# Kernel optimization log

Measured on AMD Instinct MI355X. Metric: run time of the kernel, lower is better.

## Reference

```python
import jax, jax.numpy as jnp
import numpy as np

B, L, H, D, N, R, K = 1, 2048, 2048, 4096, 16, 128, 4


def setup_inputs() -> dict:
    key = jax.random.key(0)
    ks = jax.random.split(key, 10)
    s = 0.02
    x = jax.random.normal(ks[0], (B, L, H), dtype=jnp.float32)
    W_in = jax.random.normal(ks[1], (H, 2 * D), dtype=jnp.float32) * s
    conv_w = jax.random.normal(ks[2], (K, D), dtype=jnp.float32) * s  # depthwise causal conv
    conv_b = jnp.zeros((D,), dtype=jnp.float32)
    W_x = jax.random.normal(ks[3], (D, R + 2 * N), dtype=jnp.float32) * s
    W_dt = jax.random.normal(ks[4], (R, D), dtype=jnp.float32) * (R ** -0.5)
    # dt bias initialized so softplus(b_dt) ~ dt in [1e-3, 1e-1]
    dt = jnp.exp(jax.random.uniform(ks[5], (D,)) * (np.log(0.1) - np.log(1e-3)) + np.log(1e-3))
    b_dt = dt + jnp.log(-jnp.expm1(-dt))
    A_log = jnp.broadcast_to(jnp.log(jnp.arange(1, N + 1, dtype=jnp.float32)), (D, N))
    D_param = jnp.ones((D,), dtype=jnp.float32)
    W_out = jax.random.normal(ks[6], (D, H), dtype=jnp.float32) * s
    return {"x": x, "W_in": W_in, "conv_w": conv_w, "conv_b": conv_b,
            "W_x": W_x, "W_dt": W_dt, "b_dt": b_dt, "A_log": A_log,
            "D_param": D_param, "W_out": W_out}


def _mamba_fwd(x, W_in, conv_w, conv_b, W_x, W_dt, b_dt, A_log, D_param, W_out):
    silu = jax.nn.silu
    # in_proj then chunk into hidden / gate: [B,L,D] each
    proj = x @ W_in
    hs, gate = jnp.split(proj, 2, axis=-1)
    # causal depthwise conv along sequence (pad K-1 on the left)
    hs_pad = jnp.pad(hs, ((0, 0), (K - 1, 0), (0, 0)))
    conv = sum(hs_pad[:, k:k + L, :] * conv_w[k] for k in range(K)) + conv_b
    hs = silu(conv)  # [B,L,D]
    # ssm parameters
    ssm_p = hs @ W_x  # [B,L,R+2N]
    dt_in, Bm, Cm = jnp.split(ssm_p, [R, R + N], axis=-1)
    dt = jax.nn.softplus(dt_in @ W_dt + b_dt)  # [B,L,D]
    A = -jnp.exp(A_log)  # [D,N]
    dA = jnp.exp(dt[..., None] * A)                       # [B,L,D,N]
    dBu = dt[..., None] * Bm[:, :, None, :] * hs[..., None]  # [B,L,D,N]

    def step(s, inp):
        dA_t, dBu_t, C_t = inp
        s = dA_t * s + dBu_t                 # [B,D,N]
        y = jnp.einsum('bdn,bn->bd', s, C_t)
        return s, y

    s0 = jnp.zeros((B, D, N), dtype=x.dtype)
    xs = (jnp.moveaxis(dA, 1, 0), jnp.moveaxis(dBu, 1, 0), jnp.moveaxis(Cm, 1, 0))
    _, ys = jax.lax.scan(step, s0, xs)       # [L,B,D]
    y = jnp.moveaxis(ys, 0, 1)               # [B,L,D]
    y = y + hs * D_param
    y = y * silu(gate)
    return y @ W_out                          # [B,L,H]


def reference(x, W_in, conv_w, conv_b, W_x, W_dt, b_dt, A_log, D_param, W_out):
    return _mamba_fwd(x, W_in, conv_w, conv_b, W_x, W_dt, b_dt, A_log, D_param, W_out)
```

## Files before the change

### kernel.cpp

```cpp
#include <hip/hip_runtime.h>
#include <hip/hip_bf16.h>

typedef short short8 __attribute__((ext_vector_type(8)));
typedef float floatx4 __attribute__((ext_vector_type(4)));
using bf16 = __hip_bfloat16;

static constexpr int L = 2048, H = 2048, D = 4096, NS = 16, R = 128, KC = 4;
static constexpr int CCH = 64, TCH = L / CCH;
static constexpr int KSP = 16, KCHUNK = 4096 / KSP;
static constexpr int ZOUT = 4, KOUT = 4096 / ZOUT;

__device__ __forceinline__ void g2lds16(const void* g, void* l) {
  __builtin_amdgcn_global_load_lds((const __attribute__((address_space(1))) unsigned int*)g,
                                   (__attribute__((address_space(3))) unsigned int*)l,
                                   16, 0, 0);
}

__global__ void cast_f2b(const float* __restrict__ in, bf16* __restrict__ out, int n) {
  int i = blockIdx.x * 256 + threadIdx.x;
  if (i < n) out[i] = __float2bfloat16(in[i]);
}

__global__ void transpose_cast(const float* __restrict__ in, bf16* __restrict__ out,
                               int Rr, int Cc) {
  __shared__ float tile[32][33];
  int c0 = blockIdx.x * 32, r0 = blockIdx.y * 32;
  int tx = threadIdx.x, ty = threadIdx.y;
#pragma unroll
  for (int i = 0; i < 32; i += 8)
    tile[ty + i][tx] = in[(size_t)(r0 + ty + i) * Cc + (c0 + tx)];
  __syncthreads();
#pragma unroll
  for (int i = 0; i < 32; i += 8)
    out[(size_t)(c0 + ty + i) * Rr + (r0 + tx)] = __float2bfloat16(tile[tx][ty + i]);
}

template <int MODE>
__global__ __launch_bounds__(256) void gemm_async(
    const bf16* __restrict__ A, int lda,
    const bf16* __restrict__ Bt, int ldb,
    float* __restrict__ Cf, bf16* __restrict__ Cb, int ldc, int K) {
  __shared__ short As[128 * 32];
  __shared__ short Bs[128 * 32];
  const int m0 = blockIdx.y * 128, n0 = blockIdx.x * 128;
  const int tid = threadIdx.x;
  const int lane = tid & 63;
  const int wave = tid >> 6;
  const int wm = (wave >> 1) * 64, wn = (wave & 1) * 64;
  const int lr = lane & 15, kq = lane >> 4;
  const int sr = lane >> 2, sc = (lane & 3) * 8;

  const bf16* Ab = A + (size_t)(m0 + wave * 16 + sr) * lda + sc;
  const bf16* Bb = Bt + (size_t)(n0 + wave * 16 + sr) * ldb + sc;
  short* Asw = &As[wave * 16 * 32];
  short* Bsw = &Bs[wave * 16 * 32];

  floatx4 acc[4][4];
#pragma unroll
  for (int i = 0; i < 4; i++)
#pragma unroll
    for (int j = 0; j < 4; j++)
#pragma unroll
      for (int r = 0; r < 4; r++) acc[i][j][r] = 0.f;

  for (int k0 = 0; k0 < K; k0 += 32) {
    __syncthreads();
#pragma unroll
    for (int j = 0; j < 2; j++) {
      g2lds16(Ab + (size_t)j * 64 * lda + k0, Asw + j * 64 * 32);
      g2lds16(Bb + (size_t)j * 64 * ldb + k0, Bsw + j * 64 * 32);
    }
    __syncthreads();
    short8 af[4], bfr[4];
#pragma unroll
    for (int i = 0; i < 4; i++)
      af[i] = *(const short8*)(&As[(wm + i * 16 + lr) * 32 + kq * 8]);
#pragma unroll
    for (int j = 0; j < 4; j++)
      bfr[j] = *(const short8*)(&Bs[(wn + j * 16 + lr) * 32 + kq * 8]);
#pragma unroll
    for (int i = 0; i < 4; i++)
#pragma unroll
      for (int j = 0; j < 4; j++)
        acc[i][j] = __builtin_amdgcn_mfma_f32_16x16x32_bf16(af[i], bfr[j], acc[i][j], 0, 0, 0);
  }

  const int rb = kq * 4;
#pragma unroll
  for (int i = 0; i < 4; i++)
#pragma unroll
    for (int j = 0; j < 4; j++) {
      int col = n0 + wn + j * 16 + lr;
      int row = m0 + wm + i * 16 + rb;
#pragma unroll
      for (int r = 0; r < 4; r++) {
        float v = acc[i][j][r];
        if (MODE == 0) {
          Cf[(size_t)(row + r) * ldc + col] = v;
        } else if (MODE == 1) {
          Cb[(size_t)(row + r) * ldc + col] = __float2bfloat16(v);
        } else {
          if (col < D) Cb[(size_t)(row + r) * D + col] = __float2bfloat16(v);
          else         Cf[(size_t)(row + r) * D + col - D] = v;
        }
      }
    }
}

__global__ __launch_bounds__(256) void gemm_async_splitk(
    const bf16* __restrict__ A, int lda,
    const bf16* __restrict__ Bt, int ldb,
    float* __restrict__ P, int ldc, int kch) {
  __shared__ short As[128 * 32];
  __shared__ short Bs[128 * 32];
  const int m0 = blockIdx.y * 128, n0 = blockIdx.x * 128;
  const int kbeg = blockIdx.z * kch;
  float* C = P + (size_t)blockIdx.z * L * ldc;
  const int tid = threadIdx.x;
  const int lane = tid & 63;
  const int wave = tid >> 6;
  const int wm = (wave >> 1) * 64, wn = (wave & 1) * 64;
  const int lr = lane & 15, kq = lane >> 4;
  const int sr = lane >> 2, sc = (lane & 3) * 8;

  const bf16* Ab = A + (size_t)(m0 + wave * 16 + sr) * lda + sc;
  const bf16* Bb = Bt + (size_t)(n0 + wave * 16 + sr) * ldb + sc;
  short* Asw = &As[wave * 16 * 32];
  short* Bsw = &Bs[wave * 16 * 32];

  floatx4 acc[4][4];
#pragma unroll
  for (int i = 0; i < 4; i++)
#pragma unroll
    for (int j = 0; j < 4; j++)
#pragma unroll
      for (int r = 0; r < 4; r++) acc[i][j][r] = 0.f;

  for (int k0 = kbeg; k0 < kbeg + kch; k0 += 32) {
    __syncthreads();
#pragma unroll
    for (int j = 0; j < 2; j++) {
      g2lds16(Ab + (size_t)j * 64 * lda + k0, Asw + j * 64 * 32);
      g2lds16(Bb + (size_t)j * 64 * ldb + k0, Bsw + j * 64 * 32);
    }
    __syncthreads();
    short8 af[4], bfr[4];
#pragma unroll
    for (int i = 0; i < 4; i++)
      af[i] = *(const short8*)(&As[(wm + i * 16 + lr) * 32 + kq * 8]);
#pragma unroll
    for (int j = 0; j < 4; j++)
      bfr[j] = *(const short8*)(&Bs[(wn + j * 16 + lr) * 32 + kq * 8]);
#pragma unroll
    for (int i = 0; i < 4; i++)
#pragma unroll
      for (int j = 0; j < 4; j++)
        acc[i][j] = __builtin_amdgcn_mfma_f32_16x16x32_bf16(af[i], bfr[j], acc[i][j], 0, 0, 0);
  }

  const int rb = kq * 4;
#pragma unroll
  for (int i = 0; i < 4; i++)
#pragma unroll
    for (int j = 0; j < 4; j++) {
      int col = n0 + wn + j * 16 + lr;
      int row = m0 + wm + i * 16 + rb;
#pragma unroll
      for (int r = 0; r < 4; r++)
        C[(size_t)(row + r) * ldc + col] = acc[i][j][r];
    }
}

__global__ void out_reduce(const float* __restrict__ P, float* __restrict__ out) {
  int i = blockIdx.x * 256 + threadIdx.x;
  const int LH4 = L * H / 4;
  const floatx4* P4 = (const floatx4*)P;
  floatx4 s = P4[i];
#pragma unroll
  for (int z = 1; z < ZOUT; z++) s += P4[(size_t)z * LH4 + i];
  ((floatx4*)out)[i] = s;
}

__global__ __launch_bounds__(256) void gemm_splitk(
    const bf16* __restrict__ A, int lda,
    const bf16* __restrict__ Bt, int ldb,
    float* __restrict__ P, int ldc, int N) {
  __shared__ short As[128 * 40];
  __shared__ short Bs[128 * 40];
  const int m0 = blockIdx.y * 128, n0 = blockIdx.x * 128;
  const int kbeg = blockIdx.z * KCHUNK;
  float* C = P + (size_t)blockIdx.z * L * ldc;
  const int tid = threadIdx.x;
  const int lane = tid & 63;
  const int wave = tid >> 6;
  const int wm = (wave >> 1) * 64, wn = (wave & 1) * 64;
  const int lr = lane & 15, kq = lane >> 4;
  const int srow = tid >> 2, scol = (tid & 3) * 8;

  floatx4 acc[4][4];
#pragma unroll
  for (int i = 0; i < 4; i++)
#pragma unroll
    for (int j = 0; j < 4; j++)
#pragma unroll
      for (int r = 0; r < 4; r++) acc[i][j][r] = 0.f;

  for (int k0 = kbeg; k0 < kbeg + KCHUNK; k0 += 32) {
    __syncthreads();
#pragma unroll
    for (int h = 0; h < 2; h++) {
      int r = srow + h * 64;
      short8 va = *(const short8*)((const short*)A + (size_t)(m0 + r) * lda + k0 + scol);
      *(short8*)(&As[r * 40 + scol]) = va;
    }
#pragma unroll
    for (int h = 0; h < 2; h++) {
      int r = srow + h * 64;
      short8 vb;
      if ((n0 + r) < N) {
        vb = *(const short8*)((const short*)Bt + (size_t)(n0 + r) * ldb + k0 + scol);
      } else {
#pragma unroll
        for (int q = 0; q < 8; q++) vb[q] = 0;
      }
      *(short8*)(&Bs[r * 40 + scol]) = vb;
    }
    __syncthreads();
    short8 af[4], bfr[4];
#pragma unroll
    for (int i = 0; i < 4; i++)
      af[i] = *(const short8*)(&As[(wm + i * 16 + lr) * 40 + kq * 8]);
#pragma unroll
    for (int j = 0; j < 4; j++)
      bfr[j] = *(const short8*)(&Bs[(wn + j * 16 + lr) * 40 + kq * 8]);
#pragma unroll
    for (int i = 0; i < 4; i++)
#pragma unroll
      for (int j = 0; j < 4; j++)
        acc[i][j] = __builtin_amdgcn_mfma_f32_16x16x32_bf16(af[i], bfr[j], acc[i][j], 0, 0, 0);
  }

  const int rb = kq * 4;
#pragma unroll
  for (int i = 0; i < 4; i++)
#pragma unroll
    for (int j = 0; j < 4; j++) {
      int col = n0 + wn + j * 16 + lr;
      if (col >= N) continue;
      int row = m0 + wm + i * 16 + rb;
#pragma unroll
      for (int r = 0; r < 4; r++)
        C[(size_t)(row + r) * ldc + col] = acc[i][j][r];
    }
}

__global__ void splitk_reduce(const float* __restrict__ P, float* __restrict__ ssmp,
                              bf16* __restrict__ dtin) {
  int idx = blockIdx.x * 256 + threadIdx.x;
  float s = 0.f;
#pragma unroll
  for (int z = 0; z < KSP; z++) s += P[(size_t)z * L * 160 + idx];
  ssmp[idx] = s;
  int t = idx / 160, c = idx - t * 160;
  if (c < R) dtin[t * R + c] = __float2bfloat16(s);
}

__global__ void conv_silu(const bf16* __restrict__ projh,
                          const float* __restrict__ conv_w, const float* __restrict__ conv_b,
                          bf16* __restrict__ hs_b) {
  int idx = blockIdx.x * 256 + threadIdx.x;
  int d = idx & (D - 1), t = idx >> 12;
  float acc = conv_b[d];
#pragma unroll
  for (int k = 0; k < KC; k++) {
    int tt = t + k - (KC - 1);
    if (tt >= 0) acc += __bfloat162float(projh[(size_t)tt * D + d]) * conv_w[k * D + d];
  }
  float s = acc / (1.f + __expf(-acc));
  hs_b[idx] = __float2bfloat16(s);
}

__device__ __forceinline__ float softplusf(float v) {
  return (v > 20.f) ? v : log1pf(__expf(v));
}

__global__ __launch_bounds__(256) void scan_phase1(
    const bf16* __restrict__ dtraw, const float* __restrict__ b_dt,
    const bf16* __restrict__ hs_b, const float* __restrict__ ssmp,
    const float* __restrict__ A_log,
    float* __restrict__ sdt_out, float* __restrict__ S_out) {
  const int d = blockIdx.x * 256 + threadIdx.x;
  const int c = blockIdx.y;
  float An[NS];
#pragma unroll
  for (int n = 0; n < NS; n++) An[n] = -__expf(A_log[d * NS + n]);
  const float bdt = b_dt[d];
  float s[NS];
#pragma unroll
  for (int n = 0; n < NS; n++) s[n] = 0.f;
  float sdt = 0.f;
  const int t0 = c * TCH;
#pragma unroll 2
  for (int t = t0; t < t0 + TCH; t++) {
    float dtv = softplusf(__bfloat162float(dtraw[(size_t)t * D + d]) + bdt);
    float hsv = __bfloat162float(hs_b[(size_t)t * D + d]);
    sdt += dtv;
    float u = dtv * hsv;
    const float* Bp = ssmp + (size_t)t * 160 + 128;
#pragma unroll
    for (int n = 0; n < NS; n++) {
      float dA = __expf(An[n] * dtv);
      s[n] = dA * s[n] + Bp[n] * u;
    }
  }
  sdt_out[(size_t)c * D + d] = sdt;
  float* Sp = S_out + ((size_t)c * D + d) * NS;
#pragma unroll
  for (int n = 0; n < NS; n += 4)
    *(floatx4*)(Sp + n) = *(floatx4*)(s + n);
}

__global__ __launch_bounds__(256) void scan_phase2(
    const float* __restrict__ sdt, const float* __restrict__ S,
    const float* __restrict__ A_log, float* __restrict__ I) {
  int g = blockIdx.x * 256 + threadIdx.x;
  int d = g >> 4;
  float An = -__expf(A_log[g]);
  float cur = 0.f;
  float sdt_n = sdt[d];
  float S_n = S[g];
  for (int c = 0; c < CCH; c++) {
    float sdt_c = sdt_n, S_c = S_n;
    if (c + 1 < CCH) {
      sdt_n = sdt[(size_t)(c + 1) * D + d];
      S_n = S[(size_t)(c + 1) * D * NS + g];
    }
    I[(size_t)c * D * NS + g] = cur;
    cur = __expf(An * sdt_c) * cur + S_c;
  }
}

__global__ __launch_bounds__(256) void scan_phase3(
    const bf16* __restrict__ dtraw, const float* __restrict__ b_dt,
    const bf16* __restrict__ hs_b, const float* __restrict__ ssmp,
    const float* __restrict__ gate_f, const float* __restrict__ A_log,
    const float* __restrict__ D_param, const float* __restrict__ I,
    bf16* __restrict__ y_b) {
  const int d = blockIdx.x * 256 + threadIdx.x;
  const int c = blockIdx.y;
  float An[NS];
#pragma unroll
  for (int n = 0; n < NS; n++) An[n] = -__expf(A_log[d * NS + n]);
  const float bdt = b_dt[d];
  const float Dp = D_param[d];
  float s[NS];
  const float* Ip = I + ((size_t)c * D + d) * NS;
#pragma unroll
  for (int n = 0; n < NS; n += 4)
    *(floatx4*)(s + n) = *(const floatx4*)(Ip + n);
  const int t0 = c * TCH;
#pragma unroll 2
  for (int t = t0; t < t0 + TCH; t++) {
    float dtv = softplusf(__bfloat162float(dtraw[(size_t)t * D + d]) + bdt);
    float hsv = __bfloat162float(hs_b[(size_t)t * D + d]);
    float u = dtv * hsv;
    const float* Bp = ssmp + (size_t)t * 160 + 128;
    const float* Cp = ssmp + (size_t)t * 160 + 144;
    float y = 0.f;
#pragma unroll
    for (int n = 0; n < NS; n++) {
      float dA = __expf(An[n] * dtv);
      s[n] = dA * s[n] + Bp[n] * u;
      y += s[n] * Cp[n];
    }
    float gv = gate_f[(size_t)t * D + d];
    float yv = (y + hsv * Dp) * (gv / (1.f + __expf(-gv)));
    y_b[(size_t)t * D + d] = __float2bfloat16(yv);
  }
}

extern "C" void kernel_launch(void* const* d_in, const int* in_sizes, int n_in,
                              void* d_out, int out_size, void* d_ws, size_t ws_size,
                              hipStream_t stream) {
  const float* x      = (const float*)d_in[0];
  const float* W_in   = (const float*)d_in[1];
  const float* conv_w = (const float*)d_in[2];
  const float* conv_b = (const float*)d_in[3];
  const float* W_x    = (const float*)d_in[4];
  const float* W_dt   = (const float*)d_in[5];
  const float* b_dt   = (const float*)d_in[6];
  const float* A_log  = (const float*)d_in[7];
  const float* D_par  = (const float*)d_in[8];
  const float* W_out  = (const float*)d_in[9];
  float* outp = (float*)d_out;

  char* ws = (char*)d_ws;
  size_t off = 0;
  auto alloc = [&](size_t bytes) {
    char* p = ws + off;
    off += (bytes + 255) & ~(size_t)255;
    return (void*)p;
  };
  float* gate_f  = (float*)alloc((size_t)L * D * 4);
  bf16*  hs_b    = (bf16*) alloc((size_t)L * D * 2);
  float* ssmp    = (float*)alloc((size_t)L * 160 * 4);
  bf16*  dtin_b  = (bf16*) alloc((size_t)L * R * 2);
  bf16*  dtbuf_b = (bf16*) alloc((size_t)L * D * 2);
  bf16*  y_b     = (bf16*) alloc((size_t)L * D * 2);
  bf16*  WoutT   = (bf16*) alloc((size_t)H * D * 2);
  float* sdt     = (float*)alloc((size_t)CCH * D * 4);
  float* Sbuf    = (float*)alloc((size_t)CCH * D * NS * 4);
  float* Ibuf    = (float*)alloc((size_t)CCH * D * NS * 4);
  size_t tbase = off;
  bf16*  x_b     = (bf16*) alloc((size_t)L * H * 2);
  bf16*  WinT    = (bf16*) alloc((size_t)2 * D * H * 2);
  bf16*  WxT     = (bf16*) alloc((size_t)160 * D * 2);
  bf16*  WdtT   = (bf16*) alloc((size_t)D * R * 2);
  bf16*  projh_b = (bf16*) alloc((size_t)L * D * 2);
  float* part    = (float*)alloc((size_t)KSP * L * 160 * 4);
  float* part2   = (float*)(ws + tbase);

  cast_f2b<<<(L * H) / 256, 256, 0, stream>>>(x, x_b, L * H);

  dim3 tb(32, 8);
  transpose_cast<<<dim3((2 * D) / 32, H / 32), tb, 0, stream>>>(W_in, WinT, H, 2 * D);
  transpose_cast<<<dim3(H / 32, D / 32), tb, 0, stream>>>(W_out, WoutT, D, H);
  transpose_cast<<<dim3(160 / 32, D / 32), tb, 0, stream>>>(W_x, WxT, D, 160);
  transpose_cast<<<dim3(D / 32, R / 32), tb, 0, stream>>>(W_dt, WdtT, R, D);

  gemm_async<2><<<dim3((2 * D) / 128, L / 128), 256, 0, stream>>>(
      x_b, H, WinT, H, gate_f, projh_b, D, H);
  conv_silu<<<(L * D) / 256, 256, 0, stream>>>(projh_b, conv_w, conv_b, hs_b);
  gemm_splitk<<<dim3(2, L / 128, KSP), 256, 0, stream>>>(
      hs_b, D, WxT, D, part, 160, 160);
  splitk_reduce<<<(L * 160) / 256, 256, 0, stream>>>(part, ssmp, dtin_b);
  gemm_async<1><<<dim3(D / 128, L / 128), 256, 0, stream>>>(
      dtin_b, R, WdtT, R, nullptr, dtbuf_b, D, R);

  scan_phase1<<<dim3(D / 256, CCH), 256, 0, stream>>>(
      dtbuf_b, b_dt, hs_b, ssmp, A_log, sdt, Sbuf);
  scan_phase2<<<(D * NS) / 256, 256, 0, stream>>>(sdt, Sbuf, A_log, Ibuf);
  scan_phase3<<<dim3(D / 256, CCH), 256, 0, stream>>>(
      dtbuf_b, b_dt, hs_b, ssmp, gate_f, A_log, D_par, Ibuf, y_b);

  gemm_async_splitk<<<dim3(H / 128, L / 128, ZOUT), 256, 0, stream>>>(
      y_b, D, WoutT, D, part2, H, KOUT);
  out_reduce<<<(L * H / 4) / 256, 256, 0, stream>>>(part2, outp);
}
```

Measured before the change: 538.5 us.

## Store gate in bf16 and retile output GEMM to 128x64 with 2-way split-K

The input-projection GEMM now writes the gate half as bf16 instead of fp32, which halves that write and the matching read in the scan phase-3 kernel. The output projection switches from a 128x128 tile with 4-way split-K to a 128x64 tile with 2-way split-K. This keeps the same block count but halves the partial-sum traffic and the work in the final reduce. The cost is bf16 rounding on the gate values and lower per-block data reuse in the output GEMM.

Measured after the change: 529.4 us. No clear change (-1.7%).

```diff
diff --git a/kernel.cpp b/kernel.cpp
--- a/kernel.cpp
+++ b/kernel.cpp
@@ -8,7 +8,7 @@
 static constexpr int L = 2048, H = 2048, D = 4096, NS = 16, R = 128, KC = 4;
 static constexpr int CCH = 64, TCH = L / CCH;
 static constexpr int KSP = 16, KCHUNK = 4096 / KSP;
-static constexpr int ZOUT = 4, KOUT = 4096 / ZOUT;
+static constexpr int ZOUT = 2, KOUT = 4096 / ZOUT;
 
 __device__ __forceinline__ void g2lds16(const void* g, void* l) {
   __builtin_amdgcn_global_load_lds((const __attribute__((address_space(1))) unsigned int*)g,
@@ -39,7 +39,7 @@
 __global__ __launch_bounds__(256) void gemm_async(
     const bf16* __restrict__ A, int lda,
     const bf16* __restrict__ Bt, int ldb,
-    float* __restrict__ Cf, bf16* __restrict__ Cb, int ldc, int K) {
+    bf16* __restrict__ Cb, bf16* __restrict__ Cb2, int ldc, int K) {
   __shared__ short As[128 * 32];
   __shared__ short Bs[128 * 32];
   const int m0 = blockIdx.y * 128, n0 = blockIdx.x * 128;
@@ -85,41 +85,38 @@
         acc[i][j] = __builtin_amdgcn_mfma_f32_16x16x32_bf16(af[i], bfr[j], acc[i][j], 0, 0, 0);
   }
 
+  bf16* base = Cb;
+  int coff = 0, ld = ldc;
+  if (MODE == 2) {
+    if (n0 >= D) { base = Cb2; coff = D; }
+    ld = D;
+  }
   const int rb = kq * 4;
 #pragma unroll
   for (int i = 0; i < 4; i++)
 #pragma unroll
     for (int j = 0; j < 4; j++) {
-      int col = n0 + wn + j * 16 + lr;
+      int col = n0 + wn + j * 16 + lr - coff;
       int row = m0 + wm + i * 16 + rb;
 #pragma unroll
-      for (int r = 0; r < 4; r++) {
-        float v = acc[i][j][r];
-        if (MODE == 0) {
-          Cf[(size_t)(row + r) * ldc + col] = v;
-        } else if (MODE == 1) {
-          Cb[(size_t)(row + r) * ldc + col] = __float2bfloat16(v);
-        } else {
-          if (col < D) Cb[(size_t)(row + r) * D + col] = __float2bfloat16(v);
-          else         Cf[(size_t)(row + r) * D + col - D] = v;
-        }
-      }
-    }
-}
-
-__global__ __launch_bounds__(256) void gemm_async_splitk(
+      for (int r = 0; r < 4; r++)
+        base[(size_t)(row + r) * ld + col] = __float2bfloat16(acc[i][j][r]);
+    }
+}
+
+__global__ __launch_bounds__(256) void gemm_out(
     const bf16* __restrict__ A, int lda,
     const bf16* __restrict__ Bt, int ldb,
-    float* __restrict__ P, int ldc, int kch) {
+    float* __restrict__ P, int ldc) {
   __shared__ short As[128 * 32];
-  __shared__ short Bs[128 * 32];
-  const int m0 = blockIdx.y * 128, n0 = blockIdx.x * 128;
-  const int kbeg = blockIdx.z * kch;
+  __shared__ short Bs[64 * 32];
+  const int m0 = blockIdx.y * 128, n0 = blockIdx.x * 64;
+  const int kbeg = blockIdx.z * KOUT;
   float* C = P + (size_t)blockIdx.z * L * ldc;
   const int tid = threadIdx.x;
   const int lane = tid & 63;
   const int wave = tid >> 6;
-  const int wm = (wave >> 1) * 64, wn = (wave & 1) * 64;
+  const int wm = (wave >> 1) * 64, wn = (wave & 1) * 32;
   const int lr = lane & 15, kq = lane >> 4;
   const int sr = lane >> 2, sc = (lane & 3) * 8;
 
@@ -128,41 +125,39 @@
   short* Asw = &As[wave * 16 * 32];
   short* Bsw = &Bs[wave * 16 * 32];
 
-  floatx4 acc[4][4];
-#pragma unroll
-  for (int i = 0; i < 4; i++)
-#pragma unroll
-    for (int j = 0; j < 4; j++)
+  floatx4 acc[4][2];
+#pragma unroll
+  for (int i = 0; i < 4; i++)
+#pragma unroll
+    for (int j = 0; j < 2; j++)
 #pragma unroll
       for (int r = 0; r < 4; r++) acc[i][j][r] = 0.f;
 
-  for (int k0 = kbeg; k0 < kbeg + kch; k0 += 32) {
-    __syncthreads();
+  for (int k0 = kbeg; k0 < kbeg + KOUT; k0 += 32) {
+    __syncthreads();
+    g2lds16(Ab + k0, Asw);
+    g2lds16(Ab + (size_t)64 * lda + k0, Asw + 64 * 32);
+    g2lds16(Bb + k0, Bsw);
+    __syncthreads();
+    short8 af[4], bfr[2];
+#pragma unroll
+    for (int i = 0; i < 4; i++)
+      af[i] = *(const short8*)(&As[(wm + i * 16 + lr) * 32 + kq * 8]);
+#pragma unroll
+    for (int j = 0; j < 2; j++)
+      bfr[j] = *(const short8*)(&Bs[(wn + j * 16 + lr) * 32 + kq * 8]);
+#pragma unroll
+    for (int i = 0; i < 4; i++)
+#pragma unroll
+      for (int j = 0; j < 2; j++)
+        acc[i][j] = __builtin_amdgcn_mfma_f32_16x16x32_bf16(af[i], bfr[j], acc[i][j], 0, 0, 0);
+  }
+
+  const int rb = kq * 4;
+#pragma unroll
+  for (int i = 0; i < 4; i++)
 #pragma unroll
     for (int j = 0; j < 2; j++) {
-      g2lds16(Ab + (size_t)j * 64 * lda + k0, Asw + j * 64 * 32);
-      g2lds16(Bb + (size_t)j * 64 * ldb + k0, Bsw + j * 64 * 32);
-    }
-    __syncthreads();
-    short8 af[4], bfr[4];
-#pragma unroll
-    for (int i = 0; i < 4; i++)
-      af[i] = *(const short8*)(&As[(wm + i * 16 + lr) * 32 + kq * 8]);
-#pragma unroll
-    for (int j = 0; j < 4; j++)
-      bfr[j] = *(const short8*)(&Bs[(wn + j * 16 + lr) * 32 + kq * 8]);
-#pragma unroll
-    for (int i = 0; i < 4; i++)
-#pragma unroll
-      for (int j = 0; j < 4; j++)
-        acc[i][j] = __builtin_amdgcn_mfma_f32_16x16x32_bf16(af[i], bfr[j], acc[i][j], 0, 0, 0);
-  }
-
-  const int rb = kq * 4;
-#pragma unroll
-  for (int i = 0; i < 4; i++)
-#pragma unroll
-    for (int j = 0; j < 4; j++) {
       int col = n0 + wn + j * 16 + lr;
       int row = m0 + wm + i * 16 + rb;
 #pragma unroll
@@ -343,7 +338,7 @@
 __global__ __launch_bounds__(256) void scan_phase3(
     const bf16* __restrict__ dtraw, const float* __restrict__ b_dt,
     const bf16* __restrict__ hs_b, const float* __restrict__ ssmp,
-    const float* __restrict__ gate_f, const float* __restrict__ A_log,
+    const bf16* __restrict__ gate_b, const float* __restrict__ A_log,
     const float* __restrict__ D_param, const float* __restrict__ I,
     bf16* __restrict__ y_b) {
   const int d = blockIdx.x * 256 + threadIdx.x;
@@ -373,7 +368,7 @@
       s[n] = dA * s[n] + Bp[n] * u;
       y += s[n] * Cp[n];
     }
-    float gv = gate_f[(size_t)t * D + d];
+    float gv = __bfloat162float(gate_b[(size_t)t * D + d]);
     float yv = (y + hsv * Dp) * (gv / (1.f + __expf(-gv)));
     y_b[(size_t)t * D + d] = __float2bfloat16(yv);
   }
@@ -401,7 +396,7 @@
     off += (bytes + 255) & ~(size_t)255;
     return (void*)p;
   };
-  float* gate_f  = (float*)alloc((size_t)L * D * 4);
+  bf16*  gate_b  = (bf16*) alloc((size_t)L * D * 2);
   bf16*  hs_b    = (bf16*) alloc((size_t)L * D * 2);
   float* ssmp    = (float*)alloc((size_t)L * 160 * 4);
   bf16*  dtin_b  = (bf16*) alloc((size_t)L * R * 2);
@@ -415,7 +410,7 @@
   bf16*  x_b     = (bf16*) alloc((size_t)L * H * 2);
   bf16*  WinT    = (bf16*) alloc((size_t)2 * D * H * 2);
   bf16*  WxT     = (bf16*) alloc((size_t)160 * D * 2);
-  bf16*  WdtT   = (bf16*) alloc((size_t)D * R * 2);
+  bf16*  WdtT    = (bf16*) alloc((size_t)D * R * 2);
   bf16*  projh_b = (bf16*) alloc((size_t)L * D * 2);
   float* part    = (float*)alloc((size_t)KSP * L * 160 * 4);
   float* part2   = (float*)(ws + tbase);
@@ -429,21 +424,21 @@
   transpose_cast<<<dim3(D / 32, R / 32), tb, 0, stream>>>(W_dt, WdtT, R, D);
 
   gemm_async<2><<<dim3((2 * D) / 128, L / 128), 256, 0, stream>>>(
-      x_b, H, WinT, H, gate_f, projh_b, D, H);
+      x_b, H, WinT, H, projh_b, gate_b, D, H);
   conv_silu<<<(L * D) / 256, 256, 0, stream>>>(projh_b, conv_w, conv_b, hs_b);
   gemm_splitk<<<dim3(2, L / 128, KSP), 256, 0, stream>>>(
       hs_b, D, WxT, D, part, 160, 160);
   splitk_reduce<<<(L * 160) / 256, 256, 0, stream>>>(part, ssmp, dtin_b);
   gemm_async<1><<<dim3(D / 128, L / 128), 256, 0, stream>>>(
-      dtin_b, R, WdtT, R, nullptr, dtbuf_b, D, R);
+      dtin_b, R, WdtT, R, dtbuf_b, nullptr, D, R);
 
   scan_phase1<<<dim3(D / 256, CCH), 256, 0, stream>>>(
       dtbuf_b, b_dt, hs_b, ssmp, A_log, sdt, Sbuf);
   scan_phase2<<<(D * NS) / 256, 256, 0, stream>>>(sdt, Sbuf, A_log, Ibuf);
   scan_phase3<<<dim3(D / 256, CCH), 256, 0, stream>>>(
-      dtbuf_b, b_dt, hs_b, ssmp, gate_f, A_log, D_par, Ibuf, y_b);
-
-  gemm_async_splitk<<<dim3(H / 128, L / 128, ZOUT), 256, 0, stream>>>(
-      y_b, D, WoutT, D, part2, H, KOUT);
+      dtbuf_b, b_dt, hs_b, ssmp, gate_b, A_log, D_par, Ibuf, y_b);
+
+  gemm_out<<<dim3(H / 64, L / 128, ZOUT), 256, 0, stream>>>(
+      y_b, D, WoutT, D, part2, H);
   out_reduce<<<(L * H / 4) / 256, 256, 0, stream>>>(part2, outp);
 }
```
